# Performance work log

Hardware: AMD Instinct MI355X
Metric: run time of the kernel (lower is better)

The kernel has to match this reference:

```python
import jax, jax.numpy as jnp
import numpy as np
from jax import lax

H = W = 8
N = H * W            # grid cells
D = 34               # token dim = 16 + 16 + 2
NH = 2               # attention heads
FF = 2048            # torch TransformerEncoderLayer default dim_feedforward
EPS = 1e-5


def setup_inputs():
    key = jax.random.key(0)
    ks = iter(jax.random.split(key, 64))
    rn = lambda shape, s=0.05: jax.random.normal(next(ks), shape, jnp.float32) * s
    inp = {"obs": jax.random.normal(next(ks), (2, H, W), jnp.float32), "action": 2}
    inp["conv1_w"] = rn((16, 2, 3, 3)); inp["conv1_b"] = rn((16,))
    inp["conv2_w"] = rn((16, 16, 3, 3)); inp["conv2_b"] = rn((16,))
    for l in range(2):
        p = f"l{l}_"
        inp[p + "in_w"] = rn((3 * D, D)); inp[p + "in_b"] = rn((3 * D,))
        inp[p + "out_w"] = rn((D, D)); inp[p + "out_b"] = rn((D,))
        inp[p + "ff1_w"] = rn((FF, D)); inp[p + "ff1_b"] = rn((FF,))
        inp[p + "ff2_w"] = rn((D, FF)); inp[p + "ff2_b"] = rn((D,))
        inp[p + "ln1_g"] = jnp.ones((D,)); inp[p + "ln1_b"] = jnp.zeros((D,))
        inp[p + "ln2_g"] = jnp.ones((D,)); inp[p + "ln2_b"] = jnp.zeros((D,))
    inp["act_w"] = rn((8, 4)); inp["act_b"] = rn((8,))
    inp["head_w"] = rn((16, D + 8)); inp["head_b"] = rn((16,))
    return inp


def _ln(x, g, b):
    m = x.mean(-1, keepdims=True)
    v = ((x - m) ** 2).mean(-1, keepdims=True)
    return (x - m) * lax.rsqrt(v + EPS) * g + b


def _mha(x, in_w, in_b, out_w, out_b):
    S = x.shape[0]
    hd = D // NH
    qkv = x @ in_w.T + in_b                          # [S, 3D]
    q, k, v = jnp.split(qkv, 3, axis=-1)
    q = q.reshape(S, NH, hd).transpose(1, 0, 2)      # [H, S, hd]
    k = k.reshape(S, NH, hd).transpose(1, 0, 2)
    v = v.reshape(S, NH, hd).transpose(1, 0, 2)
    attn = jax.nn.softmax(jnp.einsum('hsd,htd->hst', q, k) * (1.0 / float(np.sqrt(hd))), axis=-1)
    o = jnp.einsum('hst,htd->hsd', attn, v).transpose(1, 0, 2).reshape(S, D)
    return o @ out_w.T + out_b


def _layer(x, in_w, in_b, out_w, out_b, ff1_w, ff1_b, ff2_w, ff2_b, ln1_g, ln1_b, ln2_g, ln2_b):
    # torch default post-norm, relu activation, dropout off (eval)
    x = _ln(x + _mha(x, in_w, in_b, out_w, out_b), ln1_g, ln1_b)
    h = jax.nn.relu(x @ ff1_w.T + ff1_b) @ ff2_w.T + ff2_b
    return _ln(x + h, ln2_g, ln2_b)


def _forward(obs, conv1_w, conv1_b, conv2_w, conv2_b, layers, act_w, act_b, head_w, head_b, action):
    x = obs[None]                                    # [1, 2, H, W]
    dn = ('NCHW', 'OIHW', 'NCHW')
    x = jax.nn.relu(lax.conv_general_dilated(x, conv1_w, (1, 1), 'SAME', dimension_numbers=dn) + conv1_b[None, :, None, None])
    x = jax.nn.relu(lax.conv_general_dilated(x, conv2_w, (1, 1), 'SAME', dimension_numbers=dn) + conv2_b[None, :, None, None])
    cell = x.reshape(16, N).T                        # [N, 16]
    # vectorized pairwise relation tokens (replaces O(N^2) python loop)
    r = (jnp.arange(N) // W).astype(jnp.float32)
    c = (jnp.arange(N) % W).astype(jnp.float32)
    dx = (r[:, None] - r[None, :]) / ((H - 1) / 2.0)
    dy = (c[:, None] - c[None, :]) / ((W - 1) / 2.0)
    rel = jnp.stack([dx, dy], axis=-1)               # [N, N, 2]
    a = jnp.broadcast_to(cell[:, None, :], (N, N, 16))
    b = jnp.broadcast_to(cell[None, :, :], (N, N, 16))
    seq = jnp.concatenate([a, b, rel], axis=-1).reshape(N * N, D)
    for p in layers:
        seq = _layer(seq, *p)
    agent_idx = jnp.argmax(obs[0].reshape(-1))
    agent_tok = lax.dynamic_slice_in_dim(seq, agent_idx * N, N, 0)  # rows for agent cell
    hvec = agent_tok.mean(0)
    a_emb = jax.nn.relu(jax.nn.one_hot(action, 4, dtype=jnp.float32) @ act_w.T + act_b)
    return (jnp.concatenate([hvec, a_emb]) @ head_w.T + head_b)[None]


def reference(obs, action, conv1_w, conv1_b, conv2_w, conv2_b,
              l0_in_w, l0_in_b, l0_out_w, l0_out_b, l0_ff1_w, l0_ff1_b, l0_ff2_w, l0_ff2_b,
              l0_ln1_g, l0_ln1_b, l0_ln2_g, l0_ln2_b,
              l1_in_w, l1_in_b, l1_out_w, l1_out_b, l1_ff1_w, l1_ff1_b, l1_ff2_w, l1_ff2_b,
              l1_ln1_g, l1_ln1_b, l1_ln2_g, l1_ln2_b,
              act_w, act_b, head_w, head_b):
    layers = [
        (l0_in_w, l0_in_b, l0_out_w, l0_out_b, l0_ff1_w, l0_ff1_b, l0_ff2_w, l0_ff2_b, l0_ln1_g, l0_ln1_b, l0_ln2_g, l0_ln2_b),
        (l1_in_w, l1_in_b, l1_out_w, l1_out_b, l1_ff1_w, l1_ff1_b, l1_ff2_w, l1_ff2_b, l1_ln1_g, l1_ln1_b, l1_ln2_g, l1_ln2_b),
    ]
    return _forward(obs, conv1_w, conv1_b, conv2_w, conv2_b, layers, act_w, act_b, head_w, head_b, action)
```

## Files before the change

### kernel.cpp

```cpp
#include <hip/hip_runtime.h>
#include <math.h>

#define SEQ 4096
#define DIM 34
#define NHEAD 2
#define HD 17
#define FFDIM 2048
#define SC2 0.34990494f

#define EXP2F(x) __builtin_amdgcn_exp2f(x)
#define MFMA16(a, b, c) __builtin_amdgcn_mfma_f32_16x16x32_bf16(a, b, c, 0, 0, 0)

typedef unsigned short u16;
typedef __attribute__((ext_vector_type(8))) short bf16x8;
typedef __attribute__((ext_vector_type(4))) float f32x4;

__device__ inline u16 f2bf(float f) {
    uint32_t u = __builtin_bit_cast(uint32_t, f);
    u += 0x7fffu + ((u >> 16) & 1u);
    return (u16)(u >> 16);
}
__device__ inline uint32_t pack2(float a, float b) {
    uint32_t ua = __builtin_bit_cast(uint32_t, a);
    ua += 0x7fffu + ((ua >> 16) & 1u);
    uint32_t ub = __builtin_bit_cast(uint32_t, b);
    ub += 0x7fffu + ((ub >> 16) & 1u);
    return (ua >> 16) | (ub & 0xffff0000u);
}

#define W1B_ELEMS (FFDIM * 64)
#define W2B_ELEMS (48 * FFDIM)
#define NWCONV 448

__global__ __launch_bounds__(1024) void wm_pre(
    const float* __restrict__ obs,
    const float* __restrict__ c1w, const float* __restrict__ c1b,
    const float* __restrict__ c2w, const float* __restrict__ c2b,
    const float* __restrict__ in_w, const float* __restrict__ in_b,
    const float* __restrict__ w1a, const float* __restrict__ b1a, const float* __restrict__ w2a,
    const float* __restrict__ w1b, const float* __restrict__ b1b, const float* __restrict__ w2b,
    float* __restrict__ x, u16* __restrict__ Qb, u16* __restrict__ Kb,
    u16* __restrict__ Vc, u16* __restrict__ V16,
    u16* __restrict__ W1A, u16* __restrict__ W2A,
    u16* __restrict__ W1B, u16* __restrict__ W2B)
{
    const int tid = threadIdx.x;
    if (blockIdx.x < NWCONV) {
        int id = blockIdx.x * 1024 + tid;
        const int half = W1B_ELEMS + W2B_ELEMS;
        const float* w1 = w1a; const float* b1 = b1a; const float* w2 = w2a;
        u16* W1 = W1A; u16* W2 = W2A;
        if (id >= half) { id -= half; w1 = w1b; b1 = b1b; w2 = w2b; W1 = W1B; W2 = W2B; }
        if (id < W1B_ELEMS) {
            int n = id >> 6, c = id & 63;
            float v = (c < DIM) ? w1[n*DIM + c] : ((c == DIM) ? b1[n] : 0.f);
            W1[id] = f2bf(v);
        } else {
            int e = id - W1B_ELEMS;
            int n = e >> 11;
            float v = (n < DIM) ? w2[(n << 11) + (e & 2047)] : 0.f;
            W2[e] = f2bf(v);
        }
        return;
    }
    __shared__ float obsp[2][10][10];
    __shared__ float h1p[16][10][10];
    __shared__ float cs[64][17];
    const int sb = blockIdx.x - NWCONV;
    const int t0 = sb * 64;

    for (int e = tid; e < 200; e += 1024) ((float*)obsp)[e] = 0.f;
    for (int e = tid; e < 1600; e += 1024) ((float*)h1p)[e] = 0.f;
    __syncthreads();
    if (tid < 128) {
        int i = tid >> 6, n = tid & 63, y = n >> 3, xx = n & 7;
        obsp[i][y + 1][xx + 1] = obs[tid];
    }
    __syncthreads();
    {
        int o = tid >> 6, n = tid & 63, y = n >> 3, xx = n & 7;
        float a = c1b[o];
        #pragma unroll
        for (int i = 0; i < 2; ++i)
            #pragma unroll
            for (int ky = 0; ky < 3; ++ky)
                #pragma unroll
                for (int kx = 0; kx < 3; ++kx)
                    a = fmaf(obsp[i][y + ky][xx + kx], c1w[((o*2 + i)*3 + ky)*3 + kx], a);
        h1p[o][y + 1][xx + 1] = fmaxf(a, 0.f);
    }
    __syncthreads();
    {
        int o = tid >> 6, n = tid & 63, y = n >> 3, xx = n & 7;
        float a = c2b[o];
        #pragma unroll
        for (int i = 0; i < 16; ++i)
            #pragma unroll
            for (int ky = 0; ky < 3; ++ky)
                #pragma unroll
                for (int kx = 0; kx < 3; ++kx)
                    a = fmaf(h1p[i][y + ky][xx + kx], c2w[((o*16 + i)*3 + ky)*3 + kx], a);
        cs[n][o] = fmaxf(a, 0.f);
    }
    __syncthreads();
    for (int e = tid; e < 64 * DIM; e += 1024) {
        int tl = e / DIM, d = e % DIM;
        int t = t0 + tl, i = t >> 6, j = t & 63;
        float v;
        if (d < 16)       v = cs[i][d];
        else if (d < 32)  v = cs[j][d - 16];
        else if (d == 32) v = (float)((i >> 3) - (j >> 3)) * (1.0f / 3.5f);
        else              v = (float)((i & 7) - (j & 7)) * (1.0f / 3.5f);
        x[t0 * DIM + e] = v;
    }
    for (int ii = 0; ii < 11; ++ii) {
        int e = tid + ii * 1024;
        if (e >= 64 * 162) break;
        int t = t0 + (e & 63), slot = e >> 6;
        int i = t >> 6, j = t & 63;
        float dx = (float)((i >> 3) - (j >> 3)) * (1.0f / 3.5f);
        float dy = (float)((i & 7) - (j & 7)) * (1.0f / 3.5f);
        if (slot < 128) {
            int isK = slot >> 6, h2 = (slot >> 5) & 1, hs = slot & 31;
            float val = 0.f;
            if (hs < HD) {
                int row = isK*DIM + h2*HD + hs;
                const float* wr = in_w + row*DIM;
                float a = in_b[row];
                #pragma unroll
                for (int d = 0; d < 16; ++d) a = fmaf(cs[i][d], wr[d], a);
                #pragma unroll
                for (int d = 0; d < 16; ++d) a = fmaf(cs[j][d], wr[16 + d], a);
                a = fmaf(dx, wr[32], a);
                a = fmaf(dy, wr[33], a);
                val = isK ? a : a * SC2;
            }
            u16* dst = isK ? Kb : Qb;
            dst[(((size_t)h2*SEQ + t) << 5) + hs] = f2bf(val);
        } else {
            int s = slot - 128;
            int h2 = s >= HD, dd = s - h2*HD;
            int row = 2*DIM + h2*HD + dd;
            const float* wr = in_w + row*DIM;
            float a = in_b[row];
            #pragma unroll
            for (int d = 0; d < 16; ++d) a = fmaf(cs[i][d], wr[d], a);
            #pragma unroll
            for (int d = 0; d < 16; ++d) a = fmaf(cs[j][d], wr[16 + d], a);
            a = fmaf(dx, wr[32], a);
            a = fmaf(dy, wr[33], a);
            u16 v = f2bf(a);
            if (dd == 16) V16[h2*SEQ + t] = v;
            else {
                int c = t >> 5, g = (t >> 3) & 3, ix = t & 7;
                Vc[((((size_t)h2*128 + c)*4 + g)*16 + dd)*8 + ix] = v;
            }
        }
    }
}

__global__ __launch_bounds__(1024) void wm_attn3(const u16* __restrict__ Qb,
        const u16* __restrict__ Kb, const u16* __restrict__ Vc,
        const u16* __restrict__ V16, float* __restrict__ x,
        const float* __restrict__ ow, const float* __restrict__ obias,
        const float* __restrict__ g, const float* __restrict__ be)
{
    const int qt = blockIdx.x;
    const int tid = threadIdx.x;
    const int wv = tid >> 6, l = tid & 63;
    const int h = wv >> 3, rr = wv & 7;
    const int q = l & 15, gg = l >> 4;

    __shared__ float red[16][64][9];
    __shared__ float os[16][DIM];
    __shared__ float ys[16][DIM];
    __shared__ float stats[16][2];

    const u16* Qh = Qb + (((size_t)h*SEQ + qt*16 + q) << 5) + 8*gg;
    const u16* Kh = Kb + ((size_t)h*SEQ << 5);
    const u16* Vh = Vc + (size_t)h*128*512;
    const u16* V6 = V16 + (size_t)h*SEQ;

    const bf16x8 qf = *(const bf16x8*)Qh;
    const f32x4 zero4 = {0.f, 0.f, 0.f, 0.f};

    f32x4 olo = zero4, ohi = zero4;
    float m = -INFINITY, lsum = 0.f;

    const int srcA = q + 32*(gg & 1);
    const int srcB = srcA + 16;
    const bool hi = (gg >= 2);

    for (int it = 0; it < 8; ++it) {
        const int cA = rr*16 + it*2;
        const int k0 = cA * 32;
        bf16x8 kf0 = *(const bf16x8*)(Kh + ((size_t)(k0 + q) << 5) + 8*gg);
        bf16x8 kf1 = *(const bf16x8*)(Kh + ((size_t)(k0 + 16 + q) << 5) + 8*gg);
        bf16x8 kf2 = *(const bf16x8*)(Kh + ((size_t)(k0 + 32 + q) << 5) + 8*gg);
        bf16x8 kf3 = *(const bf16x8*)(Kh + ((size_t)(k0 + 48 + q) << 5) + 8*gg);
        f32x4 s0 = MFMA16(kf0, qf, zero4);
        f32x4 s1 = MFMA16(kf1, qf, zero4);
        f32x4 s2 = MFMA16(kf2, qf, zero4);
        f32x4 s3 = MFMA16(kf3, qf, zero4);
        float tm = fmaxf(
            fmaxf(fmaxf(fmaxf(s0[0], s0[1]), fmaxf(s0[2], s0[3])),
                  fmaxf(fmaxf(s1[0], s1[1]), fmaxf(s1[2], s1[3]))),
            fmaxf(fmaxf(fmaxf(s2[0], s2[1]), fmaxf(s2[2], s2[3])),
                  fmaxf(fmaxf(s3[0], s3[1]), fmaxf(s3[2], s3[3]))));
        tm = fmaxf(tm, __shfl_xor(tm, 16));
        tm = fmaxf(tm, __shfl_xor(tm, 32));
        float newm = fmaxf(m, tm);
        float fac = EXP2F(m - newm);
        m = newm;
        float pa0 = EXP2F(s0[0] - m), pa1 = EXP2F(s0[1] - m);
        float pa2 = EXP2F(s0[2] - m), pa3 = EXP2F(s0[3] - m);
        float pa4 = EXP2F(s1[0] - m), pa5 = EXP2F(s1[1] - m);
        float pa6 = EXP2F(s1[2] - m), pa7 = EXP2F(s1[3] - m);
        float pb0 = EXP2F(s2[0] - m), pb1 = EXP2F(s2[1] - m);
        float pb2 = EXP2F(s2[2] - m), pb3 = EXP2F(s2[3] - m);
        float pb4 = EXP2F(s3[0] - m), pb5 = EXP2F(s3[1] - m);
        float pb6 = EXP2F(s3[2] - m), pb7 = EXP2F(s3[3] - m);
        float ts = (((pa0 + pa1) + (pa2 + pa3)) + ((pa4 + pa5) + (pa6 + pa7)))
                 + (((pb0 + pb1) + (pb2 + pb3)) + ((pb4 + pb5) + (pb6 + pb7)));
        ts += __shfl_xor(ts, 16);
        ts += __shfl_xor(ts, 32);
        lsum = lsum * fac + ts;
        olo[0] *= fac; olo[1] *= fac; olo[2] *= fac; olo[3] *= fac;
        ohi[0] *= fac; ohi[1] *= fac; ohi[2] *= fac; ohi[3] *= fac;
        {
            uint32_t a0t0 = pack2(pa0, pa1), a1t0 = pack2(pa2, pa3);
            uint32_t a0t1 = pack2(pa4, pa5), a1t1 = pack2(pa6, pa7);
            uint32_t w0a = (uint32_t)__shfl((int)a0t0, srcA), w0b = (uint32_t)__shfl((int)a0t1, srcA);
            uint32_t w1a = (uint32_t)__shfl((int)a1t0, srcA), w1b = (uint32_t)__shfl((int)a1t1, srcA);
            uint32_t w2a = (uint32_t)__shfl((int)a0t0, srcB), w2b = (uint32_t)__shfl((int)a0t1, srcB);
            uint32_t w3a = (uint32_t)__shfl((int)a1t0, srcB), w3b = (uint32_t)__shfl((int)a1t1, srcB);
            union { uint32_t u[4]; bf16x8 v; } pu;
            pu.u[0] = hi ? w0b : w0a;
            pu.u[1] = hi ? w1b : w1a;
            pu.u[2] = hi ? w2b : w2a;
            pu.u[3] = hi ? w3b : w3a;
            bf16x8 vf = *(const bf16x8*)(Vh + (size_t)(cA*4 + gg)*128 + q*8);
            bf16x8 v6 = {};
            if (q == 0) v6 = *(const bf16x8*)(V6 + k0 + 8*gg);
            olo = MFMA16(vf, pu.v, olo);
            ohi = MFMA16(v6, pu.v, ohi);
        }
        {
            uint32_t a0t0 = pack2(pb0, pb1), a1t0 = pack2(pb2, pb3);
            uint32_t a0t1 = pack2(pb4, pb5), a1t1 = pack2(pb6, pb7);
            uint32_t w0a = (uint32_t)__shfl((int)a0t0, srcA), w0b = (uint32_t)__shfl((int)a0t1, srcA);
            uint32_t w1a = (uint32_t)__shfl((int)a1t0, srcA), w1b = (uint32_t)__shfl((int)a1t1, srcA);
            uint32_t w2a = (uint32_t)__shfl((int)a0t0, srcB), w2b = (uint32_t)__shfl((int)a0t1, srcB);
            uint32_t w3a = (uint32_t)__shfl((int)a1t0, srcB), w3b = (uint32_t)__shfl((int)a1t1, srcB);
            union { uint32_t u[4]; bf16x8 v; } pu;
            pu.u[0] = hi ? w0b : w0a;
            pu.u[1] = hi ? w1b : w1a;
            pu.u[2] = hi ? w2b : w2a;
            pu.u[3] = hi ? w3b : w3a;
            bf16x8 vf = *(const bf16x8*)(Vh + (size_t)((cA + 1)*4 + gg)*128 + q*8);
            bf16x8 v6 = {};
            if (q == 0) v6 = *(const bf16x8*)(V6 + k0 + 32 + 8*gg);
            olo = MFMA16(vf, pu.v, olo);
            ohi = MFMA16(v6, pu.v, ohi);
        }
    }

    {
        float* r = red[wv][l];
        r[0] = m; r[1] = lsum;
        r[2] = olo[0]; r[3] = olo[1]; r[4] = olo[2]; r[5] = olo[3];
        r[6] = ohi[0];
    }
    __syncthreads();
    if (rr == 0) {
        float M = red[wv][l][0];
        #pragma unroll
        for (int p = 1; p < 8; ++p) M = fmaxf(M, red[wv + p][l][0]);
        float lt = 0.f, o0 = 0.f, o1 = 0.f, o2 = 0.f, o3 = 0.f, o6 = 0.f;
        #pragma unroll
        for (int p = 0; p < 8; ++p) {
            float* r = red[wv + p][l];
            float fp = EXP2F(r[0] - M);
            lt += r[1]*fp;
            o0 += r[2]*fp; o1 += r[3]*fp; o2 += r[4]*fp; o3 += r[5]*fp; o6 += r[6]*fp;
        }
        float inv = 1.f / lt;
        os[q][h*HD + 4*gg + 0] = o0*inv;
        os[q][h*HD + 4*gg + 1] = o1*inv;
        os[q][h*HD + 4*gg + 2] = o2*inv;
        os[q][h*HD + 4*gg + 3] = o3*inv;
        if (gg == 0) os[q][h*HD + 16] = o6*inv;
    }
    __syncthreads();
    for (int e = tid; e < 16 * DIM; e += 1024) {
        int tt = e / DIM, d = e % DIM;
        const float* wr = ow + d*DIM;
        float acc = obias[d];
        #pragma unroll
        for (int k = 0; k < DIM; ++k) acc = fmaf(os[tt][k], wr[k], acc);
        ys[tt][d] = x[(size_t)(qt*16 + tt)*DIM + d] + acc;
    }
    __syncthreads();
    if (tid < 16) {
        float s1 = 0.f, s2 = 0.f;
        #pragma unroll
        for (int d = 0; d < DIM; ++d) { float v = ys[tid][d]; s1 += v; s2 += v*v; }
        float mean = s1 * (1.0f / DIM);
        float var  = s2 * (1.0f / DIM) - mean*mean;
        stats[tid][0] = mean;
        stats[tid][1] = rsqrtf(var + 1e-5f);
    }
    __syncthreads();
    for (int e = tid; e < 16 * DIM; e += 1024) {
        int tt = e / DIM, d = e % DIM;
        x[(size_t)(qt*16 + tt)*DIM + d] = (ys[tt][d] - stats[tt][0]) * stats[tt][1] * g[d] + be[d];
    }
}

__global__ __launch_bounds__(1024) void wm_ff3(float* __restrict__ x,
        const u16* __restrict__ W1b, const u16* __restrict__ W2b,
        const float* __restrict__ b2, const float* __restrict__ g,
        const float* __restrict__ be,
        const float* __restrict__ in_w, const float* __restrict__ in_b,
        u16* __restrict__ Qb, u16* __restrict__ Kb,
        u16* __restrict__ Vc, u16* __restrict__ V16, int do_qkv)
{
    __shared__ u16 Hs[16][16][128];
    __shared__ float red[16][16][52];
    __shared__ float ys[16][DIM];
    __shared__ float stats[16][2];
    const int tid = threadIdx.x, wv = tid >> 6, l = tid & 63;
    const int q = l & 15, g4 = l >> 4;
    const int t0 = blockIdx.x * 16;

    const float* xr = x + (size_t)(t0 + q) * DIM;
    union { uint32_t u[4]; bf16x8 v; } a0, a1;
    #pragma unroll
    for (int j = 0; j < 4; ++j)
        a0.u[j] = pack2(xr[g4*8 + 2*j], xr[g4*8 + 2*j + 1]);
    a1.u[0] = 0; a1.u[1] = 0; a1.u[2] = 0; a1.u[3] = 0;
    if (g4 == 0) {
        a1.u[0] = pack2(xr[32], xr[33]);
        a1.u[1] = pack2(1.0f, 0.f);
    }
    const f32x4 zero4 = {0.f, 0.f, 0.f, 0.f};

    const int hb = wv * 128;
    #pragma unroll
    for (int nt = 0; nt < 8; ++nt) {
        const u16* brow = W1b + (size_t)(hb + nt*16 + q) * 64 + g4*8;
        bf16x8 b0 = *(const bf16x8*)brow;
        bf16x8 b1f = *(const bf16x8*)(brow + 32);
        f32x4 c = MFMA16(a0.v, b0, zero4);
        c = MFMA16(a1.v, b1f, c);
        #pragma unroll
        for (int r = 0; r < 4; ++r) {
            int mm = 4*g4 + r;
            int byte = ((nt*16 + q) * 2) ^ ((mm & 7) << 4);
            *(u16*)((char*)&Hs[wv][mm][0] + byte) = f2bf(fmaxf(c[r], 0.f));
        }
    }
    asm volatile("s_waitcnt lgkmcnt(0)" ::: "memory");
    __builtin_amdgcn_sched_barrier(0);
    f32x4 acc0 = zero4, acc1 = zero4, acc2 = zero4;
    #pragma unroll
    for (int ks = 0; ks < 4; ++ks) {
        int byte = (ks*64 + g4*16) ^ ((q & 7) << 4);
        bf16x8 af = *(const bf16x8*)((char*)&Hs[wv][q][0] + byte);
        const u16* bp = W2b + (size_t)q * FFDIM + hb + ks*32 + g4*8;
        acc0 = MFMA16(af, *(const bf16x8*)bp, acc0);
        acc1 = MFMA16(af, *(const bf16x8*)(bp + 16*FFDIM), acc1);
        acc2 = MFMA16(af, *(const bf16x8*)(bp + 32*FFDIM), acc2);
    }
    #pragma unroll
    for (int r = 0; r < 4; ++r) {
        red[wv][4*g4 + r][q]      = acc0[r];
        red[wv][4*g4 + r][16 + q] = acc1[r];
        red[wv][4*g4 + r][32 + q] = acc2[r];
    }
    __syncthreads();
    for (int e = tid; e < 16*DIM; e += 1024) {
        int tt = e / DIM, d = e % DIM;
        float v = x[(size_t)(t0 + tt)*DIM + d] + b2[d];
        #pragma unroll
        for (int w = 0; w < 16; ++w) v += red[w][tt][d];
        ys[tt][d] = v;
    }
    __syncthreads();
    if (tid < 16) {
        float s1 = 0.f, s2 = 0.f;
        #pragma unroll
        for (int d = 0; d < DIM; ++d) { float v = ys[tid][d]; s1 += v; s2 += v * v; }
        float mean = s1 * (1.0f / DIM);
        float var  = s2 * (1.0f / DIM) - mean * mean;
        stats[tid][0] = mean;
        stats[tid][1] = rsqrtf(var + 1e-5f);
    }
    __syncthreads();
    for (int e = tid; e < 16*DIM; e += 1024) {
        int tt = e / DIM, d = e % DIM;
        float v = (ys[tt][d] - stats[tt][0]) * stats[tt][1] * g[d] + be[d];
        x[(size_t)(t0 + tt)*DIM + d] = v;
        ys[tt][d] = v;
    }
    if (do_qkv) {
        __syncthreads();
        #pragma unroll
        for (int ii = 0; ii < 2; ++ii) {
            int e = tid + ii*1024;
            if (e < 16*102) {
                int r = e >> 4, tt = e & 15;
                const float* wr = in_w + r*DIM;
                float a = in_b[r];
                #pragma unroll
                for (int d = 0; d < DIM; ++d) a = fmaf(ys[tt][d], wr[d], a);
                int tg = t0 + tt;
                if (r < 68) {
                    int rq = (r < 34) ? r : r - 34;
                    int h2 = rq >= HD, hs = rq - h2*HD;
                    u16 v = f2bf((r < 34) ? a*SC2 : a);
                    u16* dst = (r < 34) ? Qb : Kb;
                    dst[(((size_t)h2*SEQ + tg) << 5) + hs] = v;
                } else {
                    int rv = r - 68;
                    int h2 = rv >= HD, dd = rv - h2*HD;
                    u16 v = f2bf(a);
                    if (dd == 16) V16[h2*SEQ + tg] = v;
                    else {
                        int c = tg >> 5, gg = (tg >> 3) & 3, ix = tg & 7;
                        Vc[((((size_t)h2*128 + c)*4 + gg)*16 + dd)*8 + ix] = v;
                    }
                }
            }
        }
    }
}

__global__ __launch_bounds__(64) void wm_final(const float* __restrict__ x,
        const float* __restrict__ obs, const int* __restrict__ action,
        const float* __restrict__ aw, const float* __restrict__ ab,
        const float* __restrict__ hw, const float* __restrict__ hb,
        float* __restrict__ out)
{
    __shared__ float hv[DIM];
    __shared__ float saemb[8];
    __shared__ int sai;
    const int tid = threadIdx.x;
    {
        float v = obs[tid];
        float mx = v;
        for (int off = 32; off; off >>= 1) mx = fmaxf(mx, __shfl_xor(mx, off));
        unsigned long long mask = __ballot(v == mx);
        if (tid == 0) sai = (int)(__ffsll(mask) - 1);
    }
    if (tid < 8) {
        int act = *action;
        saemb[tid] = fmaxf(aw[tid*4 + act] + ab[tid], 0.f);
    }
    __syncthreads();
    const int ai = sai;
    if (tid < DIM) {
        float s = 0.f;
        for (int r = 0; r < 64; ++r) s += x[(size_t)(ai*64 + r)*DIM + tid];
        hv[tid] = s * (1.0f / 64.0f);
    }
    __syncthreads();
    if (tid < 16) {
        float a = hb[tid];
        #pragma unroll
        for (int d = 0; d < DIM; ++d) a = fmaf(hv[d], hw[tid*42 + d], a);
        #pragma unroll
        for (int j = 0; j < 8; ++j) a = fmaf(saemb[j], hw[tid*42 + DIM + j], a);
        out[tid] = a;
    }
}

extern "C" void kernel_launch(void* const* d_in, const int* in_sizes, int n_in,
                              void* d_out, int out_size, void* d_ws, size_t ws_size,
                              hipStream_t stream)
{
    const float* obs    = (const float*)d_in[0];
    const int*   action = (const int*)  d_in[1];
    const float* c1w = (const float*)d_in[2];
    const float* c1b = (const float*)d_in[3];
    const float* c2w = (const float*)d_in[4];
    const float* c2b = (const float*)d_in[5];
    const float* aw  = (const float*)d_in[30];
    const float* ab  = (const float*)d_in[31];
    const float* hw  = (const float*)d_in[32];
    const float* hb  = (const float*)d_in[33];

    float* ws   = (float*)d_ws;
    float* x    = ws + 1056;
    float* o    = x + SEQ * DIM;
    u16*   Qb   = (u16*)(o + SEQ * DIM);
    u16*   Kb   = Qb + 2 * SEQ * 32;
    u16*   Vc   = Kb + 2 * SEQ * 32;
    u16*   V16  = Vc + 2 * 128 * 512;
    u16*   W1b0 = V16 + 2 * SEQ;
    u16*   W2b0 = W1b0 + W1B_ELEMS;
    u16*   W1b1 = W2b0 + W2B_ELEMS;
    u16*   W2b1 = W1b1 + W1B_ELEMS;

    wm_pre<<<NWCONV + 64, 1024, 0, stream>>>(
        obs, c1w, c1b, c2w, c2b,
        (const float*)d_in[6], (const float*)d_in[7],
        (const float*)d_in[10], (const float*)d_in[11], (const float*)d_in[12],
        (const float*)d_in[22], (const float*)d_in[23], (const float*)d_in[24],
        x, Qb, Kb, Vc, V16, W1b0, W2b0, W1b1, W2b1);

    wm_attn3<<<SEQ / 16, 1024, 0, stream>>>(Qb, Kb, Vc, V16, x,
        (const float*)d_in[8], (const float*)d_in[9],
        (const float*)d_in[14], (const float*)d_in[15]);

    wm_ff3<<<SEQ / 16, 1024, 0, stream>>>(x, W1b0, W2b0,
        (const float*)d_in[13], (const float*)d_in[16], (const float*)d_in[17],
        (const float*)d_in[18], (const float*)d_in[19],
        Qb, Kb, Vc, V16, 1);

    wm_attn3<<<SEQ / 16, 1024, 0, stream>>>(Qb, Kb, Vc, V16, x,
        (const float*)d_in[20], (const float*)d_in[21],
        (const float*)d_in[26], (const float*)d_in[27]);

    wm_ff3<<<SEQ / 16, 1024, 0, stream>>>(x, W1b1, W2b1,
        (const float*)d_in[25], (const float*)d_in[28], (const float*)d_in[29],
        (const float*)d_in[18], (const float*)d_in[19],
        Qb, Kb, Vc, V16, 0);

    wm_final<<<1, 64, 0, stream>>>(x, obs, action, aw, ab, hw, hb, (float*)d_out);
}
```

Baseline: 102.9 us.

## Fuse all stages into one cooperative persistent kernel with grid syncs

Replaces the six separate launches (pre, two attention, two feed-forward, final) with a single cooperative kernel of 256 blocks that separates stages with grid.sync(). Each block keeps its 16-token activation tile and its Q projections in LDS across phases, so only K/V and the final x go through global memory. A shared-memory union lets the phases reuse one LDS buffer. The aim is to remove launch gaps and global round-trips of x and Q. In exchange it depends on all 256 large blocks being co-resident, and it pays grid-wide barrier costs.

```diff
diff --git a/kernel.cpp b/kernel.cpp
--- a/kernel.cpp
+++ b/kernel.cpp
@@ -1,5 +1,8 @@
 #include <hip/hip_runtime.h>
+#include <hip/hip_cooperative_groups.h>
 #include <math.h>
+
+namespace cg = cooperative_groups;
 
 #define SEQ 4096
 #define DIM 34
@@ -30,158 +33,41 @@
 
 #define W1B_ELEMS (FFDIM * 64)
 #define W2B_ELEMS (48 * FFDIM)
-#define NWCONV 448
-
-__global__ __launch_bounds__(1024) void wm_pre(
-    const float* __restrict__ obs,
-    const float* __restrict__ c1w, const float* __restrict__ c1b,
-    const float* __restrict__ c2w, const float* __restrict__ c2b,
-    const float* __restrict__ in_w, const float* __restrict__ in_b,
-    const float* __restrict__ w1a, const float* __restrict__ b1a, const float* __restrict__ w2a,
-    const float* __restrict__ w1b, const float* __restrict__ b1b, const float* __restrict__ w2b,
-    float* __restrict__ x, u16* __restrict__ Qb, u16* __restrict__ Kb,
-    u16* __restrict__ Vc, u16* __restrict__ V16,
-    u16* __restrict__ W1A, u16* __restrict__ W2A,
-    u16* __restrict__ W1B, u16* __restrict__ W2B)
-{
-    const int tid = threadIdx.x;
-    if (blockIdx.x < NWCONV) {
-        int id = blockIdx.x * 1024 + tid;
-        const int half = W1B_ELEMS + W2B_ELEMS;
-        const float* w1 = w1a; const float* b1 = b1a; const float* w2 = w2a;
-        u16* W1 = W1A; u16* W2 = W2A;
-        if (id >= half) { id -= half; w1 = w1b; b1 = b1b; w2 = w2b; W1 = W1B; W2 = W2B; }
-        if (id < W1B_ELEMS) {
-            int n = id >> 6, c = id & 63;
-            float v = (c < DIM) ? w1[n*DIM + c] : ((c == DIM) ? b1[n] : 0.f);
-            W1[id] = f2bf(v);
-        } else {
-            int e = id - W1B_ELEMS;
-            int n = e >> 11;
-            float v = (n < DIM) ? w2[(n << 11) + (e & 2047)] : 0.f;
-            W2[e] = f2bf(v);
-        }
-        return;
-    }
-    __shared__ float obsp[2][10][10];
-    __shared__ float h1p[16][10][10];
-    __shared__ float cs[64][17];
-    const int sb = blockIdx.x - NWCONV;
-    const int t0 = sb * 64;
-
-    for (int e = tid; e < 200; e += 1024) ((float*)obsp)[e] = 0.f;
-    for (int e = tid; e < 1600; e += 1024) ((float*)h1p)[e] = 0.f;
-    __syncthreads();
-    if (tid < 128) {
-        int i = tid >> 6, n = tid & 63, y = n >> 3, xx = n & 7;
-        obsp[i][y + 1][xx + 1] = obs[tid];
-    }
-    __syncthreads();
-    {
-        int o = tid >> 6, n = tid & 63, y = n >> 3, xx = n & 7;
-        float a = c1b[o];
-        #pragma unroll
-        for (int i = 0; i < 2; ++i)
-            #pragma unroll
-            for (int ky = 0; ky < 3; ++ky)
-                #pragma unroll
-                for (int kx = 0; kx < 3; ++kx)
-                    a = fmaf(obsp[i][y + ky][xx + kx], c1w[((o*2 + i)*3 + ky)*3 + kx], a);
-        h1p[o][y + 1][xx + 1] = fmaxf(a, 0.f);
-    }
-    __syncthreads();
-    {
-        int o = tid >> 6, n = tid & 63, y = n >> 3, xx = n & 7;
-        float a = c2b[o];
-        #pragma unroll
-        for (int i = 0; i < 16; ++i)
-            #pragma unroll
-            for (int ky = 0; ky < 3; ++ky)
-                #pragma unroll
-                for (int kx = 0; kx < 3; ++kx)
-                    a = fmaf(h1p[i][y + ky][xx + kx], c2w[((o*16 + i)*3 + ky)*3 + kx], a);
-        cs[n][o] = fmaxf(a, 0.f);
-    }
-    __syncthreads();
-    for (int e = tid; e < 64 * DIM; e += 1024) {
-        int tl = e / DIM, d = e % DIM;
-        int t = t0 + tl, i = t >> 6, j = t & 63;
-        float v;
-        if (d < 16)       v = cs[i][d];
-        else if (d < 32)  v = cs[j][d - 16];
-        else if (d == 32) v = (float)((i >> 3) - (j >> 3)) * (1.0f / 3.5f);
-        else              v = (float)((i & 7) - (j & 7)) * (1.0f / 3.5f);
-        x[t0 * DIM + e] = v;
-    }
-    for (int ii = 0; ii < 11; ++ii) {
-        int e = tid + ii * 1024;
-        if (e >= 64 * 162) break;
-        int t = t0 + (e & 63), slot = e >> 6;
-        int i = t >> 6, j = t & 63;
-        float dx = (float)((i >> 3) - (j >> 3)) * (1.0f / 3.5f);
-        float dy = (float)((i & 7) - (j & 7)) * (1.0f / 3.5f);
-        if (slot < 128) {
-            int isK = slot >> 6, h2 = (slot >> 5) & 1, hs = slot & 31;
-            float val = 0.f;
-            if (hs < HD) {
-                int row = isK*DIM + h2*HD + hs;
-                const float* wr = in_w + row*DIM;
-                float a = in_b[row];
-                #pragma unroll
-                for (int d = 0; d < 16; ++d) a = fmaf(cs[i][d], wr[d], a);
-                #pragma unroll
-                for (int d = 0; d < 16; ++d) a = fmaf(cs[j][d], wr[16 + d], a);
-                a = fmaf(dx, wr[32], a);
-                a = fmaf(dy, wr[33], a);
-                val = isK ? a : a * SC2;
-            }
-            u16* dst = isK ? Kb : Qb;
-            dst[(((size_t)h2*SEQ + t) << 5) + hs] = f2bf(val);
-        } else {
-            int s = slot - 128;
-            int h2 = s >= HD, dd = s - h2*HD;
-            int row = 2*DIM + h2*HD + dd;
-            const float* wr = in_w + row*DIM;
-            float a = in_b[row];
-            #pragma unroll
-            for (int d = 0; d < 16; ++d) a = fmaf(cs[i][d], wr[d], a);
-            #pragma unroll
-            for (int d = 0; d < 16; ++d) a = fmaf(cs[j][d], wr[16 + d], a);
-            a = fmaf(dx, wr[32], a);
-            a = fmaf(dy, wr[33], a);
-            u16 v = f2bf(a);
-            if (dd == 16) V16[h2*SEQ + t] = v;
-            else {
-                int c = t >> 5, g = (t >> 3) & 3, ix = t & 7;
-                Vc[((((size_t)h2*128 + c)*4 + g)*16 + dd)*8 + ix] = v;
-            }
-        }
-    }
-}
-
-__global__ __launch_bounds__(1024) void wm_attn3(const u16* __restrict__ Qb,
+
+union USm {
+    struct { float obsp[2][10][10]; float h1p[16][10][10]; float cs[64][17]; } pre;
+    struct { float red[16][64][9]; float os[16][DIM]; float ys[16][DIM]; float stats[16][2]; } at;
+    struct { u16 Hs[16][16][128]; float red[16][16][52]; float ys[16][DIM]; float stats[16][2]; } ff;
+};
+
+struct MegaArgs {
+    const float *obs; const int *action;
+    const float *c1w, *c1b, *c2w, *c2b;
+    const float *in_w0, *in_b0, *ow0, *ob0, *b2_0, *ln1g0, *ln1b0, *ln2g0, *ln2b0;
+    const float *in_w1, *in_b1, *ow1, *ob1, *b2_1, *ln1g1, *ln1b1, *ln2g1, *ln2b1;
+    const float *w1_0, *b1_0, *w2_0, *w1_1, *b1_1, *w2_1;
+    const float *aw, *ab, *hw, *hb;
+    float *x; u16 *Kb, *Vc, *V16, *W1b0, *W2b0, *W1b1, *W2b1;
+    float *out;
+};
+
+__device__ __forceinline__ void attn_phase(USm& s, float (*xt)[DIM + 1],
+        u16 (*Qs)[16][32],
         const u16* __restrict__ Kb, const u16* __restrict__ Vc,
-        const u16* __restrict__ V16, float* __restrict__ x,
+        const u16* __restrict__ V16,
         const float* __restrict__ ow, const float* __restrict__ obias,
         const float* __restrict__ g, const float* __restrict__ be)
 {
-    const int qt = blockIdx.x;
     const int tid = threadIdx.x;
     const int wv = tid >> 6, l = tid & 63;
     const int h = wv >> 3, rr = wv & 7;
     const int q = l & 15, gg = l >> 4;
 
-    __shared__ float red[16][64][9];
-    __shared__ float os[16][DIM];
-    __shared__ float ys[16][DIM];
-    __shared__ float stats[16][2];
-
-    const u16* Qh = Qb + (((size_t)h*SEQ + qt*16 + q) << 5) + 8*gg;
     const u16* Kh = Kb + ((size_t)h*SEQ << 5);
     const u16* Vh = Vc + (size_t)h*128*512;
     const u16* V6 = V16 + (size_t)h*SEQ;
 
-    const bf16x8 qf = *(const bf16x8*)Qh;
+    const bf16x8 qf = *(const bf16x8*)(&Qs[h][q][8*gg]);
     const f32x4 zero4 = {0.f, 0.f, 0.f, 0.f};
 
     f32x4 olo = zero4, ohi = zero4;
@@ -266,30 +152,30 @@
     }
 
     {
-        float* r = red[wv][l];
+        float* r = s.at.red[wv][l];
         r[0] = m; r[1] = lsum;
         r[2] = olo[0]; r[3] = olo[1]; r[4] = olo[2]; r[5] = olo[3];
         r[6] = ohi[0];
     }
     __syncthreads();
     if (rr == 0) {
-        float M = red[wv][l][0];
-        #pragma unroll
-        for (int p = 1; p < 8; ++p) M = fmaxf(M, red[wv + p][l][0]);
+        float M = s.at.red[wv][l][0];
+        #pragma unroll
+        for (int p = 1; p < 8; ++p) M = fmaxf(M, s.at.red[wv + p][l][0]);
         float lt = 0.f, o0 = 0.f, o1 = 0.f, o2 = 0.f, o3 = 0.f, o6 = 0.f;
         #pragma unroll
         for (int p = 0; p < 8; ++p) {
-            float* r = red[wv + p][l];
+            float* r = s.at.red[wv + p][l];
             float fp = EXP2F(r[0] - M);
             lt += r[1]*fp;
             o0 += r[2]*fp; o1 += r[3]*fp; o2 += r[4]*fp; o3 += r[5]*fp; o6 += r[6]*fp;
         }
         float inv = 1.f / lt;
-        os[q][h*HD + 4*gg + 0] = o0*inv;
-        os[q][h*HD + 4*gg + 1] = o1*inv;
-        os[q][h*HD + 4*gg + 2] = o2*inv;
-        os[q][h*HD + 4*gg + 3] = o3*inv;
-        if (gg == 0) os[q][h*HD + 16] = o6*inv;
+        s.at.os[q][h*HD + 4*gg + 0] = o0*inv;
+        s.at.os[q][h*HD + 4*gg + 1] = o1*inv;
+        s.at.os[q][h*HD + 4*gg + 2] = o2*inv;
+        s.at.os[q][h*HD + 4*gg + 3] = o3*inv;
+        if (gg == 0) s.at.os[q][h*HD + 16] = o6*inv;
     }
     __syncthreads();
     for (int e = tid; e < 16 * DIM; e += 1024) {
@@ -297,50 +183,46 @@
         const float* wr = ow + d*DIM;
         float acc = obias[d];
         #pragma unroll
-        for (int k = 0; k < DIM; ++k) acc = fmaf(os[tt][k], wr[k], acc);
-        ys[tt][d] = x[(size_t)(qt*16 + tt)*DIM + d] + acc;
+        for (int k = 0; k < DIM; ++k) acc = fmaf(s.at.os[tt][k], wr[k], acc);
+        s.at.ys[tt][d] = xt[tt][d] + acc;
     }
     __syncthreads();
     if (tid < 16) {
         float s1 = 0.f, s2 = 0.f;
         #pragma unroll
-        for (int d = 0; d < DIM; ++d) { float v = ys[tid][d]; s1 += v; s2 += v*v; }
+        for (int d = 0; d < DIM; ++d) { float v = s.at.ys[tid][d]; s1 += v; s2 += v*v; }
         float mean = s1 * (1.0f / DIM);
         float var  = s2 * (1.0f / DIM) - mean*mean;
-        stats[tid][0] = mean;
-        stats[tid][1] = rsqrtf(var + 1e-5f);
+        s.at.stats[tid][0] = mean;
+        s.at.stats[tid][1] = rsqrtf(var + 1e-5f);
     }
     __syncthreads();
     for (int e = tid; e < 16 * DIM; e += 1024) {
         int tt = e / DIM, d = e % DIM;
-        x[(size_t)(qt*16 + tt)*DIM + d] = (ys[tt][d] - stats[tt][0]) * stats[tt][1] * g[d] + be[d];
-    }
+        xt[tt][d] = (s.at.ys[tt][d] - s.at.stats[tt][0]) * s.at.stats[tt][1] * g[d] + be[d];
+    }
+    __syncthreads();
 }
 
-__global__ __launch_bounds__(1024) void wm_ff3(float* __restrict__ x,
+__device__ __forceinline__ void ff_phase(USm& s, float (*xt)[DIM + 1],
+        u16 (*Qs)[16][32], int t0,
         const u16* __restrict__ W1b, const u16* __restrict__ W2b,
         const float* __restrict__ b2, const float* __restrict__ g,
         const float* __restrict__ be,
         const float* __restrict__ in_w, const float* __restrict__ in_b,
-        u16* __restrict__ Qb, u16* __restrict__ Kb,
-        u16* __restrict__ Vc, u16* __restrict__ V16, int do_qkv)
+        u16* __restrict__ Kb, u16* __restrict__ Vc, u16* __restrict__ V16,
+        float* __restrict__ x, int do_qkv, int store_x)
 {
-    __shared__ u16 Hs[16][16][128];
-    __shared__ float red[16][16][52];
-    __shared__ float ys[16][DIM];
-    __shared__ float stats[16][2];
     const int tid = threadIdx.x, wv = tid >> 6, l = tid & 63;
     const int q = l & 15, g4 = l >> 4;
-    const int t0 = blockIdx.x * 16;
-
-    const float* xr = x + (size_t)(t0 + q) * DIM;
+
     union { uint32_t u[4]; bf16x8 v; } a0, a1;
     #pragma unroll
     for (int j = 0; j < 4; ++j)
-        a0.u[j] = pack2(xr[g4*8 + 2*j], xr[g4*8 + 2*j + 1]);
+        a0.u[j] = pack2(xt[q][g4*8 + 2*j], xt[q][g4*8 + 2*j + 1]);
     a1.u[0] = 0; a1.u[1] = 0; a1.u[2] = 0; a1.u[3] = 0;
     if (g4 == 0) {
-        a1.u[0] = pack2(xr[32], xr[33]);
+        a1.u[0] = pack2(xt[q][32], xt[q][33]);
         a1.u[1] = pack2(1.0f, 0.f);
     }
     const f32x4 zero4 = {0.f, 0.f, 0.f, 0.f};
@@ -357,7 +239,7 @@
         for (int r = 0; r < 4; ++r) {
             int mm = 4*g4 + r;
             int byte = ((nt*16 + q) * 2) ^ ((mm & 7) << 4);
-            *(u16*)((char*)&Hs[wv][mm][0] + byte) = f2bf(fmaxf(c[r], 0.f));
+            *(u16*)((char*)&s.ff.Hs[wv][mm][0] + byte) = f2bf(fmaxf(c[r], 0.f));
         }
     }
     asm volatile("s_waitcnt lgkmcnt(0)" ::: "memory");
@@ -366,7 +248,7 @@
     #pragma unroll
     for (int ks = 0; ks < 4; ++ks) {
         int byte = (ks*64 + g4*16) ^ ((q & 7) << 4);
-        bf16x8 af = *(const bf16x8*)((char*)&Hs[wv][q][0] + byte);
+        bf16x8 af = *(const bf16x8*)((char*)&s.ff.Hs[wv][q][0] + byte);
         const u16* bp = W2b + (size_t)q * FFDIM + hb + ks*32 + g4*8;
         acc0 = MFMA16(af, *(const bf16x8*)bp, acc0);
         acc1 = MFMA16(af, *(const bf16x8*)(bp + 16*FFDIM), acc1);
@@ -374,104 +256,214 @@
     }
     #pragma unroll
     for (int r = 0; r < 4; ++r) {
-        red[wv][4*g4 + r][q]      = acc0[r];
-        red[wv][4*g4 + r][16 + q] = acc1[r];
-        red[wv][4*g4 + r][32 + q] = acc2[r];
+        s.ff.red[wv][4*g4 + r][q]      = acc0[r];
+        s.ff.red[wv][4*g4 + r][16 + q] = acc1[r];
+        s.ff.red[wv][4*g4 + r][32 + q] = acc2[r];
     }
     __syncthreads();
     for (int e = tid; e < 16*DIM; e += 1024) {
         int tt = e / DIM, d = e % DIM;
-        float v = x[(size_t)(t0 + tt)*DIM + d] + b2[d];
-        #pragma unroll
-        for (int w = 0; w < 16; ++w) v += red[w][tt][d];
-        ys[tt][d] = v;
+        float v = xt[tt][d] + b2[d];
+        #pragma unroll
+        for (int w = 0; w < 16; ++w) v += s.ff.red[w][tt][d];
+        s.ff.ys[tt][d] = v;
     }
     __syncthreads();
     if (tid < 16) {
         float s1 = 0.f, s2 = 0.f;
         #pragma unroll
-        for (int d = 0; d < DIM; ++d) { float v = ys[tid][d]; s1 += v; s2 += v * v; }
+        for (int d = 0; d < DIM; ++d) { float v = s.ff.ys[tid][d]; s1 += v; s2 += v * v; }
         float mean = s1 * (1.0f / DIM);
         float var  = s2 * (1.0f / DIM) - mean * mean;
-        stats[tid][0] = mean;
-        stats[tid][1] = rsqrtf(var + 1e-5f);
+        s.ff.stats[tid][0] = mean;
+        s.ff.stats[tid][1] = rsqrtf(var + 1e-5f);
     }
     __syncthreads();
     for (int e = tid; e < 16*DIM; e += 1024) {
         int tt = e / DIM, d = e % DIM;
-        float v = (ys[tt][d] - stats[tt][0]) * stats[tt][1] * g[d] + be[d];
-        x[(size_t)(t0 + tt)*DIM + d] = v;
-        ys[tt][d] = v;
-    }
+        float v = (s.ff.ys[tt][d] - s.ff.stats[tt][0]) * s.ff.stats[tt][1] * g[d] + be[d];
+        xt[tt][d] = v;
+        if (store_x) x[(size_t)(t0 + tt)*DIM + d] = v;
+    }
+    __syncthreads();
     if (do_qkv) {
-        __syncthreads();
-        #pragma unroll
-        for (int ii = 0; ii < 2; ++ii) {
-            int e = tid + ii*1024;
-            if (e < 16*102) {
-                int r = e >> 4, tt = e & 15;
-                const float* wr = in_w + r*DIM;
-                float a = in_b[r];
-                #pragma unroll
-                for (int d = 0; d < DIM; ++d) a = fmaf(ys[tt][d], wr[d], a);
-                int tg = t0 + tt;
-                if (r < 68) {
-                    int rq = (r < 34) ? r : r - 34;
-                    int h2 = rq >= HD, hs = rq - h2*HD;
-                    u16 v = f2bf((r < 34) ? a*SC2 : a);
-                    u16* dst = (r < 34) ? Qb : Kb;
-                    dst[(((size_t)h2*SEQ + tg) << 5) + hs] = v;
-                } else {
-                    int rv = r - 68;
-                    int h2 = rv >= HD, dd = rv - h2*HD;
-                    u16 v = f2bf(a);
-                    if (dd == 16) V16[h2*SEQ + tg] = v;
-                    else {
-                        int c = tg >> 5, gg = (tg >> 3) & 3, ix = tg & 7;
-                        Vc[((((size_t)h2*128 + c)*4 + gg)*16 + dd)*8 + ix] = v;
-                    }
+        for (int e = tid; e < 16*102; e += 1024) {
+            int r = e >> 4, tt = e & 15;
+            const float* wr = in_w + r*DIM;
+            float a = in_b[r];
+            #pragma unroll
+            for (int d = 0; d < DIM; ++d) a = fmaf(xt[tt][d], wr[d], a);
+            int tg = t0 + tt;
+            if (r < 34) {
+                int h2 = r >= HD, hs = r - h2*HD;
+                Qs[h2][tt][hs] = f2bf(a * SC2);
+            } else if (r < 68) {
+                int rq = r - 34;
+                int h2 = rq >= HD, hs = rq - h2*HD;
+                Kb[(((size_t)h2*SEQ + tg) << 5) + hs] = f2bf(a);
+            } else {
+                int rv = r - 68;
+                int h2 = rv >= HD, dd = rv - h2*HD;
+                u16 v = f2bf(a);
+                if (dd == 16) V16[h2*SEQ + tg] = v;
+                else {
+                    int c = tg >> 5, gg = (tg >> 3) & 3, ix = tg & 7;
+                    Vc[((((size_t)h2*128 + c)*4 + gg)*16 + dd)*8 + ix] = v;
                 }
             }
         }
+        __syncthreads();
     }
 }
 
-__global__ __launch_bounds__(64) void wm_final(const float* __restrict__ x,
-        const float* __restrict__ obs, const int* __restrict__ action,
-        const float* __restrict__ aw, const float* __restrict__ ab,
-        const float* __restrict__ hw, const float* __restrict__ hb,
-        float* __restrict__ out)
+__global__ __launch_bounds__(1024) void wm_mega(MegaArgs A)
 {
+    __shared__ USm sm;
+    __shared__ float xt[16][DIM + 1];
+    __shared__ u16 Qs[NHEAD][16][32];
     __shared__ float hv[DIM];
     __shared__ float saemb[8];
     __shared__ int sai;
+
     const int tid = threadIdx.x;
+    const int t0 = blockIdx.x * 16;
+    cg::grid_group grid = cg::this_grid();
+
     {
-        float v = obs[tid];
+        const int half = W1B_ELEMS + W2B_ELEMS;
+        for (int e = tid; e < 1792; e += 1024) {
+            int id = blockIdx.x * 1792 + e;
+            const float* w1 = A.w1_0; const float* b1 = A.b1_0; const float* w2 = A.w2_0;
+            u16* W1 = A.W1b0; u16* W2 = A.W2b0;
+            if (id >= half) { id -= half; w1 = A.w1_1; b1 = A.b1_1; w2 = A.w2_1; W1 = A.W1b1; W2 = A.W2b1; }
+            if (id < W1B_ELEMS) {
+                int n = id >> 6, c = id & 63;
+                float v = (c < DIM) ? w1[n*DIM + c] : ((c == DIM) ? b1[n] : 0.f);
+                W1[id] = f2bf(v);
+            } else {
+                int e2 = id - W1B_ELEMS;
+                int n = e2 >> 11;
+                float v = (n < DIM) ? w2[(n << 11) + (e2 & 2047)] : 0.f;
+                W2[e2] = f2bf(v);
+            }
+        }
+    }
+    for (int e = tid; e < 200; e += 1024) ((float*)sm.pre.obsp)[e] = 0.f;
+    for (int e = tid; e < 1600; e += 1024) ((float*)sm.pre.h1p)[e] = 0.f;
+    __syncthreads();
+    if (tid < 128) {
+        int i = tid >> 6, n = tid & 63, y = n >> 3, xx = n & 7;
+        sm.pre.obsp[i][y + 1][xx + 1] = A.obs[tid];
+    }
+    __syncthreads();
+    {
+        int o = tid >> 6, n = tid & 63, y = n >> 3, xx = n & 7;
+        float a = A.c1b[o];
+        #pragma unroll
+        for (int i = 0; i < 2; ++i)
+            #pragma unroll
+            for (int ky = 0; ky < 3; ++ky)
+                #pragma unroll
+                for (int kx = 0; kx < 3; ++kx)
+                    a = fmaf(sm.pre.obsp[i][y + ky][xx + kx], A.c1w[((o*2 + i)*3 + ky)*3 + kx], a);
+        sm.pre.h1p[o][y + 1][xx + 1] = fmaxf(a, 0.f);
+    }
+    __syncthreads();
+    {
+        int o = tid >> 6, n = tid & 63, y = n >> 3, xx = n & 7;
+        float a = A.c2b[o];
+        #pragma unroll
+        for (int i = 0; i < 16; ++i)
+            #pragma unroll
+            for (int ky = 0; ky < 3; ++ky)
+                #pragma unroll
+                for (int kx = 0; kx < 3; ++kx)
+                    a = fmaf(sm.pre.h1p[i][y + ky][xx + kx], A.c2w[((o*16 + i)*3 + ky)*3 + kx], a);
+        sm.pre.cs[n][o] = fmaxf(a, 0.f);
+    }
+    __syncthreads();
+    for (int e = tid; e < 16 * DIM; e += 1024) {
+        int tl = e / DIM, d = e % DIM;
+        int t = t0 + tl, i = t >> 6, j = t & 63;
+        float v;
+        if (d < 16)       v = sm.pre.cs[i][d];
+        else if (d < 32)  v = sm.pre.cs[j][d - 16];
+        else if (d == 32) v = (float)((i >> 3) - (j >> 3)) * (1.0f / 3.5f);
+        else              v = (float)((i & 7) - (j & 7)) * (1.0f / 3.5f);
+        xt[tl][d] = v;
+    }
+    for (int e = tid; e < 2*16*15; e += 1024) {
+        int h2 = e / 240, r2 = e % 240;
+        int tt = r2 / 15, c = 17 + r2 % 15;
+        Qs[h2][tt][c] = 0;
+        A.Kb[(((size_t)h2*SEQ + t0 + tt) << 5) + c] = 0;
+    }
+    __syncthreads();
+    for (int e = tid; e < 16*102; e += 1024) {
+        int r = e >> 4, tt = e & 15;
+        const float* wr = A.in_w0 + r*DIM;
+        float a = A.in_b0[r];
+        #pragma unroll
+        for (int d = 0; d < DIM; ++d) a = fmaf(xt[tt][d], wr[d], a);
+        int tg = t0 + tt;
+        if (r < 34) {
+            int h2 = r >= HD, hs = r - h2*HD;
+            Qs[h2][tt][hs] = f2bf(a * SC2);
+        } else if (r < 68) {
+            int rq = r - 34;
+            int h2 = rq >= HD, hs = rq - h2*HD;
+            A.Kb[(((size_t)h2*SEQ + tg) << 5) + hs] = f2bf(a);
+        } else {
+            int rv = r - 68;
+            int h2 = rv >= HD, dd = rv - h2*HD;
+            u16 v = f2bf(a);
+            if (dd == 16) A.V16[h2*SEQ + tg] = v;
+            else {
+                int c = tg >> 5, gg = (tg >> 3) & 3, ix = tg & 7;
+                A.Vc[((((size_t)h2*128 + c)*4 + gg)*16 + dd)*8 + ix] = v;
+            }
+        }
+    }
+
+    grid.sync();
+    attn_phase(sm, xt, Qs, A.Kb, A.Vc, A.V16, A.ow0, A.ob0, A.ln1g0, A.ln1b0);
+    ff_phase(sm, xt, Qs, t0, A.W1b0, A.W2b0, A.b2_0, A.ln2g0, A.ln2b0,
+             A.in_w1, A.in_b1, A.Kb, A.Vc, A.V16, A.x, 1, 0);
+
+    grid.sync();
+    attn_phase(sm, xt, Qs, A.Kb, A.Vc, A.V16, A.ow1, A.ob1, A.ln1g1, A.ln1b1);
+    ff_phase(sm, xt, Qs, t0, A.W1b1, A.W2b1, A.b2_1, A.ln2g1, A.ln2b1,
+             A.in_w1, A.in_b1, A.Kb, A.Vc, A.V16, A.x, 0, 1);
+
+    grid.sync();
+    if (blockIdx.x != 0) return;
+    if (tid < 64) {
+        float v = A.obs[tid];
         float mx = v;
         for (int off = 32; off; off >>= 1) mx = fmaxf(mx, __shfl_xor(mx, off));
         unsigned long long mask = __ballot(v == mx);
         if (tid == 0) sai = (int)(__ffsll(mask) - 1);
     }
-    if (tid < 8) {
-        int act = *action;
-        saemb[tid] = fmaxf(aw[tid*4 + act] + ab[tid], 0.f);
+    if (tid >= 64 && tid < 72) {
+        int k = tid - 64;
+        int act = *A.action;
+        saemb[k] = fmaxf(A.aw[k*4 + act] + A.ab[k], 0.f);
     }
     __syncthreads();
     const int ai = sai;
     if (tid < DIM) {
-        float s = 0.f;
-        for (int r = 0; r < 64; ++r) s += x[(size_t)(ai*64 + r)*DIM + tid];
-        hv[tid] = s * (1.0f / 64.0f);
+        float sacc = 0.f;
+        for (int r = 0; r < 64; ++r) sacc += A.x[(size_t)(ai*64 + r)*DIM + tid];
+        hv[tid] = sacc * (1.0f / 64.0f);
     }
     __syncthreads();
     if (tid < 16) {
-        float a = hb[tid];
-        #pragma unroll
-        for (int d = 0; d < DIM; ++d) a = fmaf(hv[d], hw[tid*42 + d], a);
-        #pragma unroll
-        for (int j = 0; j < 8; ++j) a = fmaf(saemb[j], hw[tid*42 + DIM + j], a);
-        out[tid] = a;
+        float a = A.hb[tid];
+        #pragma unroll
+        for (int d = 0; d < DIM; ++d) a = fmaf(hv[d], A.hw[tid*42 + d], a);
+        #pragma unroll
+        for (int j = 0; j < 8; ++j) a = fmaf(saemb[j], A.hw[tid*42 + DIM + j], a);
+        A.out[tid] = a;
     }
 }
 
@@ -479,22 +471,9 @@
                               void* d_out, int out_size, void* d_ws, size_t ws_size,
                               hipStream_t stream)
 {
-    const float* obs    = (const float*)d_in[0];
-    const int*   action = (const int*)  d_in[1];
-    const float* c1w = (const float*)d_in[2];
-    const float* c1b = (const float*)d_in[3];
-    const float* c2w = (const float*)d_in[4];
-    const float* c2b = (const float*)d_in[5];
-    const float* aw  = (const float*)d_in[30];
-    const float* ab  = (const float*)d_in[31];
-    const float* hw  = (const float*)d_in[32];
-    const float* hb  = (const float*)d_in[33];
-
     float* ws   = (float*)d_ws;
-    float* x    = ws + 1056;
-    float* o    = x + SEQ * DIM;
-    u16*   Qb   = (u16*)(o + SEQ * DIM);
-    u16*   Kb   = Qb + 2 * SEQ * 32;
+    float* x    = ws;
+    u16*   Kb   = (u16*)(x + SEQ * DIM);
     u16*   Vc   = Kb + 2 * SEQ * 32;
     u16*   V16  = Vc + 2 * 128 * 512;
     u16*   W1b0 = V16 + 2 * SEQ;
@@ -502,30 +481,30 @@
     u16*   W1b1 = W2b0 + W2B_ELEMS;
     u16*   W2b1 = W1b1 + W1B_ELEMS;
 
-    wm_pre<<<NWCONV + 64, 1024, 0, stream>>>(
-        obs, c1w, c1b, c2w, c2b,
-        (const float*)d_in[6], (const float*)d_in[7],
-        (const float*)d_in[10], (const float*)d_in[11], (const float*)d_in[12],
-        (const float*)d_in[22], (const float*)d_in[23], (const float*)d_in[24],
-        x, Qb, Kb, Vc, V16, W1b0, W2b0, W1b1, W2b1);
-
-    wm_attn3<<<SEQ / 16, 1024, 0, stream>>>(Qb, Kb, Vc, V16, x,
-        (const float*)d_in[8], (const float*)d_in[9],
-        (const float*)d_in[14], (const float*)d_in[15]);
-
-    wm_ff3<<<SEQ / 16, 1024, 0, stream>>>(x, W1b0, W2b0,
-        (const float*)d_in[13], (const float*)d_in[16], (const float*)d_in[17],
-        (const float*)d_in[18], (const float*)d_in[19],
-        Qb, Kb, Vc, V16, 1);
-
-    wm_attn3<<<SEQ / 16, 1024, 0, stream>>>(Qb, Kb, Vc, V16, x,
-        (const float*)d_in[20], (const float*)d_in[21],
-        (const float*)d_in[26], (const float*)d_in[27]);
-
-    wm_ff3<<<SEQ / 16, 1024, 0, stream>>>(x, W1b1, W2b1,
-        (const float*)d_in[25], (const float*)d_in[28], (const float*)d_in[29],
-        (const float*)d_in[18], (const float*)d_in[19],
-        Qb, Kb, Vc, V16, 0);
-
-    wm_final<<<1, 64, 0, stream>>>(x, obs, action, aw, ab, hw, hb, (float*)d_out);
+    MegaArgs A;
+    A.obs    = (const float*)d_in[0];
+    A.action = (const int*)  d_in[1];
+    A.c1w = (const float*)d_in[2];  A.c1b = (const float*)d_in[3];
+    A.c2w = (const float*)d_in[4];  A.c2b = (const float*)d_in[5];
+    A.in_w0 = (const float*)d_in[6];  A.in_b0 = (const float*)d_in[7];
+    A.ow0   = (const float*)d_in[8];  A.ob0   = (const float*)d_in[9];
+    A.w1_0  = (const float*)d_in[10]; A.b1_0  = (const float*)d_in[11];
+    A.w2_0  = (const float*)d_in[12]; A.b2_0  = (const float*)d_in[13];
+    A.ln1g0 = (const float*)d_in[14]; A.ln1b0 = (const float*)d_in[15];
+    A.ln2g0 = (const float*)d_in[16]; A.ln2b0 = (const float*)d_in[17];
+    A.in_w1 = (const float*)d_in[18]; A.in_b1 = (const float*)d_in[19];
+    A.ow1   = (const float*)d_in[20]; A.ob1   = (const float*)d_in[21];
+    A.w1_1  = (const float*)d_in[22]; A.b1_1  = (const float*)d_in[23];
+    A.w2_1  = (const float*)d_in[24]; A.b2_1  = (const float*)d_in[25];
+    A.ln1g1 = (const float*)d_in[26]; A.ln1b1 = (const float*)d_in[27];
+    A.ln2g1 = (const float*)d_in[28]; A.ln2b1 = (const float*)d_in[29];
+    A.aw = (const float*)d_in[30]; A.ab = (const float*)d_in[31];
+    A.hw = (const float*)d_in[32]; A.hb = (const float*)d_in[33];
+    A.x = x; A.Kb = Kb; A.Vc = Vc; A.V16 = V16;
+    A.W1b0 = W1b0; A.W2b0 = W2b0; A.W1b1 = W1b1; A.W2b1 = W2b1;
+    A.out = (float*)d_out;
+
+    void* kargs[] = { &A };
+    hipLaunchCooperativeKernel(reinterpret_cast<void*>(wm_mega),
+                               dim3(SEQ / 16), dim3(1024), kargs, 0, stream);
 }
```

New measurement: 186.7 us. 1.81x slower.
